# Kernel optimization log

Hardware: AMD Instinct MI355X
Metric: run time of the kernel (lower is better)

Reference implementation:

```python
import jax, jax.numpy as jnp
import numpy as np

EPS_COS = 1e-8
EPS_SHARP = 1e-16


def setup_inputs() -> dict:
    key = jax.random.key(0)
    k1, k2, k3, k4 = jax.random.split(key, 4)
    B, H, R, C, M = 512, 512, 2048, 64, 3
    out_dim = 3 * C + 2 * M + 4  # 202
    h = jax.random.normal(k1, (B, H), dtype=jnp.float32)
    prev_w = jax.random.uniform(k2, (B, R), dtype=jnp.float32)
    prev_w = prev_w / prev_w.sum(axis=1, keepdims=True)  # valid focus distribution
    memory = jax.random.normal(k3, (B, R, C), dtype=jnp.float32)
    fc_w = jax.random.normal(k4, (out_dim, H), dtype=jnp.float32) * 0.05
    fc_b = jnp.zeros((out_dim,), dtype=jnp.float32)
    return {"h": h, "prev_w": prev_w, "memory": memory, "fc_w": fc_w, "fc_b": fc_b}


def _write_head(h, prev_w, memory, fc_w, fc_b):
    B, R, C = memory.shape
    total = fc_w.shape[0]
    shift_len = total - 3 * C - 3          # 2*max_shift + 1
    m = (shift_len - 1) // 2               # max_shift

    z = h @ fc_w.T + fc_b                  # [B, total]
    sizes = [C, 1, 1, shift_len, 1, C, C]
    offs = np.cumsum([0] + sizes)
    k     = jnp.tanh(z[:, offs[0]:offs[1]])                 # [B, C]
    beta  = jax.nn.softplus(z[:, offs[1]:offs[2]])          # [B, 1]
    g     = jax.nn.sigmoid(z[:, offs[2]:offs[3]])           # [B, 1]
    s     = jax.nn.softmax(z[:, offs[3]:offs[4]], axis=1)   # [B, 2m+1]
    gamma = jax.nn.softplus(z[:, offs[4]:offs[5]]) + 1.0    # [B, 1]
    e     = jax.nn.sigmoid(z[:, offs[5]:offs[6]])           # [B, C]
    a     = jnp.tanh(z[:, offs[6]:offs[7]])                 # [B, C]

    # content addressing: cosine similarity of k vs each memory row
    num = jnp.einsum('bc,brc->br', k, memory)
    k_n = jnp.maximum(jnp.linalg.norm(k, axis=1, keepdims=True), EPS_COS)   # [B,1]
    m_n = jnp.maximum(jnp.linalg.norm(memory, axis=2), EPS_COS)             # [B,R]
    w_c = jax.nn.softmax(beta * (num / (k_n * m_n)), axis=1)                # [B,R]

    # gated interpolation
    w_g = g * w_c + (1.0 - g) * prev_w                                      # [B,R]

    # circular shift (per-sample cross-correlation, O(B*R*(2m+1)))
    unrolled = jnp.concatenate([w_g[:, -m:], w_g, w_g[:, :m]], axis=1)      # [B, R+2m]
    windows = jnp.stack([unrolled[:, j:j + R] for j in range(2 * m + 1)], axis=1)  # [B,2m+1,R]
    w_s = jnp.einsum('bjr,bj->br', windows, s)                              # [B,R]

    # sharpen
    w_p = jnp.power(w_s, gamma)
    w = w_p / (w_p.sum(axis=1, keepdims=True) + EPS_SHARP)                  # [B,R]

    # erase + write (fused)
    wE = w[:, :, None]                                                      # [B,R,1]
    new_mem = memory * (1.0 - wE * e[:, None, :]) + wE * a[:, None, :]      # [B,R,C]
    return w, new_mem


def reference(h, prev_w, memory, fc_w, fc_b):
    return _write_head(h, prev_w, memory, fc_w, fc_b)
```

## Files before the change

kernel.cpp:

```cpp
#include <hip/hip_runtime.h>
#include <math.h>

#define BB 512
#define HH 512
#define RR 2048
#define CC 64
#define OUTD 202
#define PSTRIDE 208
#define K_OFF 0
#define E_OFF 64
#define A_OFF 128
#define S_OFF 192
#define COMBO_OFF 199
#define G_OFF 200
#define GAMMA_OFF 201

#define PART_STRIDE 224

typedef float f32x4 __attribute__((ext_vector_type(4)));

__device__ __forceinline__ float softplusf_(float x) {
    return (x > 20.f) ? x : log1pf(expf(x));
}
__device__ __forceinline__ float sigmoidf_(float x) {
    return 1.f / (1.f + expf(-x));
}

__global__ __launch_bounds__(256) void params_part_kernel(
    const float* __restrict__ h, const float* __restrict__ fc_w,
    float* __restrict__ part)
{
    __shared__ float h_sh[8][128];
    const int tid = threadIdx.x;
    const int bg = blockIdx.x >> 2;
    const int hq = blockIdx.x & 3;
    const int b0 = bg * 8;
    const int h0 = hq * 128;

    for (int idx = tid; idx < 8 * 128; idx += 256) {
        int j = idx >> 7, i = idx & 127;
        h_sh[j][i] = h[(size_t)(b0 + j) * HH + h0 + i];
    }
    __syncthreads();

    if (tid < OUTD) {
        float acc[8];
        #pragma unroll
        for (int j = 0; j < 8; ++j) acc[j] = 0.f;
        const float4* wr = (const float4*)(fc_w + (size_t)tid * HH + h0);
        #pragma unroll 4
        for (int i4 = 0; i4 < 32; ++i4) {
            float4 wv = wr[i4];
            int i = i4 * 4;
            #pragma unroll
            for (int j = 0; j < 8; ++j) {
                acc[j] = fmaf(wv.x, h_sh[j][i + 0], acc[j]);
                acc[j] = fmaf(wv.y, h_sh[j][i + 1], acc[j]);
                acc[j] = fmaf(wv.z, h_sh[j][i + 2], acc[j]);
                acc[j] = fmaf(wv.w, h_sh[j][i + 3], acc[j]);
            }
        }
        #pragma unroll
        for (int j = 0; j < 8; ++j) {
            part[((size_t)(b0 + j) * 4 + hq) * PART_STRIDE + tid] = acc[j];
        }
    }
}

__global__ __launch_bounds__(256) void params_combine_kernel(
    const float* __restrict__ part, const float* __restrict__ fc_b,
    float* __restrict__ pw)
{
    __shared__ float z_sh[80];
    const int b = blockIdx.x;
    const int tid = threadIdx.x;
    float* p = pw + (size_t)b * PSTRIDE;

    if (tid < OUTD) {
        const float* q = part + (size_t)b * 4 * PART_STRIDE + tid;
        float z = q[0] + q[PART_STRIDE] + q[2 * PART_STRIDE]
                + q[3 * PART_STRIDE] + fc_b[tid];
        if (tid < 74) z_sh[tid] = z;
        if (tid < 64)                      p[K_OFF + tid] = tanhf(z);
        else if (tid == 65)                p[G_OFF] = sigmoidf_(z);
        else if (tid == 73)                p[GAMMA_OFF] = softplusf_(z) + 1.f;
        else if (tid >= 74 && tid < 138)   p[E_OFF + (tid - 74)] = sigmoidf_(z);
        else if (tid >= 138)               p[A_OFF + (tid - 138)] = tanhf(z);
    }
    __syncthreads();

    if (tid < 64) {
        float kv = tanhf(z_sh[tid]);
        float ss = kv * kv;
        #pragma unroll
        for (int m = 1; m < 64; m <<= 1) ss += __shfl_xor(ss, m, 64);
        if (tid == 0) {
            float kn = fmaxf(sqrtf(ss), 1e-8f);
            float beta = softplusf_(z_sh[64]);
            p[COMBO_OFF] = beta / kn;
            float mx = -1e30f;
            #pragma unroll
            for (int q = 0; q < 7; ++q) mx = fmaxf(mx, z_sh[66 + q]);
            float ev[7], se = 0.f;
            #pragma unroll
            for (int q = 0; q < 7; ++q) {
                ev[q] = __expf(z_sh[66 + q] - mx);
                se += ev[q];
            }
            float inv = 1.f / se;
            #pragma unroll
            for (int q = 0; q < 7; ++q) p[S_OFF + q] = ev[q] * inv;
        }
    }
}

__device__ __forceinline__ float block_reduce_sum4(float v, float* red) {
    #pragma unroll
    for (int m = 1; m < 64; m <<= 1) v += __shfl_xor(v, m, 64);
    int wid = threadIdx.x >> 6;
    if ((threadIdx.x & 63) == 0) red[wid] = v;
    __syncthreads();
    float x = red[0] + red[1] + red[2] + red[3];
    __syncthreads();
    return x;
}

__global__ __launch_bounds__(256) void score_kernel(
    const float* __restrict__ memory, const float* __restrict__ pw,
    float* __restrict__ sc, float* __restrict__ esum)
{
    __shared__ float red[4];
    const int tid = threadIdx.x;
    const int b = blockIdx.x >> 2;
    const int rbase = (blockIdx.x & 3) * 512;
    const int lane16 = tid & 15;
    const int rgrp = tid >> 4;
    const float* p = pw + (size_t)b * PSTRIDE;
    const float4 k4 = *(const float4*)(p + K_OFF + lane16 * 4);
    const float combo = p[COMBO_OFF];
    const float* memb = memory + (size_t)b * RR * CC;

    float lsum = 0.f;
    #pragma unroll 8
    for (int i = 0; i < 32; ++i) {
        int r = rbase + i * 16 + rgrp;
        float4 m4 = *(const float4*)(memb + (size_t)r * CC + lane16 * 4);
        float num = m4.x * k4.x + m4.y * k4.y + m4.z * k4.z + m4.w * k4.w;
        float ssq = m4.x * m4.x + m4.y * m4.y + m4.z * m4.z + m4.w * m4.w;
        #pragma unroll
        for (int m = 1; m < 16; m <<= 1) {
            num += __shfl_xor(num, m, 64);
            ssq += __shfl_xor(ssq, m, 64);
        }
        if (lane16 == 0) {
            float mn = fmaxf(sqrtf(ssq), 1e-8f);
            float ev = __expf(combo * num / mn);
            sc[(size_t)b * RR + r] = ev;
            lsum += ev;
        }
    }
    float bs = block_reduce_sum4(lsum, red);
    if (tid == 0) esum[blockIdx.x] = bs;
}

__device__ __forceinline__ float block_reduce_sum16(float v, float* red) {
    #pragma unroll
    for (int m = 1; m < 64; m <<= 1) v += __shfl_xor(v, m, 64);
    int wid = threadIdx.x >> 6;
    if ((threadIdx.x & 63) == 0) red[wid] = v;
    __syncthreads();
    if (threadIdx.x < 16) {
        float x = red[threadIdx.x];
        #pragma unroll
        for (int m = 1; m < 16; m <<= 1) x += __shfl_xor(x, m, 64);
        if (threadIdx.x == 0) red[0] = x;
    }
    __syncthreads();
    float r = red[0];
    __syncthreads();
    return r;
}

__global__ __launch_bounds__(1024) void wu_kernel(
    const float* __restrict__ memory, const float* __restrict__ sc,
    const float* __restrict__ esum, const float* __restrict__ prev_w,
    const float* __restrict__ pw, float* __restrict__ out_w,
    float* __restrict__ out_mem)
{
    __shared__ float wg[RR];
    __shared__ float wps[RR];
    __shared__ float red[16];

    const int b = blockIdx.x;
    const int tid = threadIdx.x;
    const float* p = pw + (size_t)b * PSTRIDE;
    const float g = p[G_OFF];
    const float gamma = p[GAMMA_OFF];
    const float s0 = p[S_OFF + 0], s1 = p[S_OFF + 1], s2 = p[S_OFF + 2],
                s3 = p[S_OFF + 3], s4 = p[S_OFF + 4], s5 = p[S_OFF + 5],
                s6 = p[S_OFF + 6];
    const float* eb = esum + (size_t)b * 4;
    const float se = eb[0] + eb[1] + eb[2] + eb[3];
    const float gi = g / se, omg = 1.f - g;

    {
        const int r2 = tid * 2;
        float2 ev = *(const float2*)(sc + (size_t)b * RR + r2);
        float2 pv = *(const float2*)(prev_w + (size_t)b * RR + r2);
        wg[r2]     = gi * ev.x + omg * pv.x;
        wg[r2 + 1] = gi * ev.y + omg * pv.y;
    }
    __syncthreads();

    float lp = 0.f;
    {
        const int r2 = tid * 2;
        #pragma unroll
        for (int q = 0; q < 2; ++q) {
            int r = r2 + q;
            float acc = s0 * wg[(r - 3) & (RR - 1)]
                      + s1 * wg[(r - 2) & (RR - 1)]
                      + s2 * wg[(r - 1) & (RR - 1)]
                      + s3 * wg[r]
                      + s4 * wg[(r + 1) & (RR - 1)]
                      + s5 * wg[(r + 2) & (RR - 1)]
                      + s6 * wg[(r + 3) & (RR - 1)];
            float v = __powf(acc, gamma);
            wps[r] = v;
            lp += v;
        }
    }
    const float ps = block_reduce_sum16(lp, red);
    const float invp = 1.f / (ps + 1e-16f);

    {
        const int r2 = tid * 2;
        float w0 = wps[r2] * invp;
        float w1 = wps[r2 + 1] * invp;
        wg[r2] = w0;
        wg[r2 + 1] = w1;
        *(float2*)(out_w + (size_t)b * RR + r2) = make_float2(w0, w1);
    }
    __syncthreads();

    const int lane8 = tid & 7;
    const int rgrp = tid >> 3;
    const f32x4 ea = *(const f32x4*)(p + E_OFF + lane8 * 8);
    const f32x4 eb2 = *(const f32x4*)(p + E_OFF + lane8 * 8 + 4);
    const f32x4 aa = *(const f32x4*)(p + A_OFF + lane8 * 8);
    const f32x4 ab = *(const f32x4*)(p + A_OFF + lane8 * 8 + 4);
    const float* memb = memory + (size_t)b * RR * CC;
    float* omb = out_mem + (size_t)b * RR * CC;

    #pragma unroll
    for (int mi = 0; mi < 4; ++mi) {
        f32x4 ma[4], mb[4];
        float wv[4];
        #pragma unroll
        for (int j = 0; j < 4; ++j) {
            int r = (mi * 4 + j) * 128 + rgrp;
            const f32x4* mp = (const f32x4*)(memb + (size_t)r * CC + lane8 * 8);
            ma[j] = mp[0];
            mb[j] = mp[1];
            wv[j] = wg[r];
        }
        #pragma unroll
        for (int j = 0; j < 4; ++j) {
            int r = (mi * 4 + j) * 128 + rgrp;
            f32x4 oa, ob;
            oa.x = ma[j].x * (1.f - wv[j] * ea.x) + wv[j] * aa.x;
            oa.y = ma[j].y * (1.f - wv[j] * ea.y) + wv[j] * aa.y;
            oa.z = ma[j].z * (1.f - wv[j] * ea.z) + wv[j] * aa.z;
            oa.w = ma[j].w * (1.f - wv[j] * ea.w) + wv[j] * aa.w;
            ob.x = mb[j].x * (1.f - wv[j] * eb2.x) + wv[j] * ab.x;
            ob.y = mb[j].y * (1.f - wv[j] * eb2.y) + wv[j] * ab.y;
            ob.z = mb[j].z * (1.f - wv[j] * eb2.z) + wv[j] * ab.z;
            ob.w = mb[j].w * (1.f - wv[j] * eb2.w) + wv[j] * ab.w;
            f32x4* op = (f32x4*)(omb + (size_t)r * CC + lane8 * 8);
            op[0] = oa;
            op[1] = ob;
        }
    }
}

extern "C" void kernel_launch(void* const* d_in, const int* in_sizes, int n_in,
                              void* d_out, int out_size, void* d_ws, size_t ws_size,
                              hipStream_t stream) {
    const float* h      = (const float*)d_in[0];
    const float* prev_w = (const float*)d_in[1];
    const float* memory = (const float*)d_in[2];
    const float* fc_w   = (const float*)d_in[3];
    const float* fc_b   = (const float*)d_in[4];

    float* pw      = (float*)d_ws;
    float* out_w   = (float*)d_out;
    float* out_mem = out_w + (size_t)BB * RR;

    const size_t pw_f   = (size_t)BB * PSTRIDE;
    const size_t br_f   = (size_t)BB * RR;
    const size_t es_f   = (size_t)BB * 4;
    const size_t part_f = (size_t)BB * 4 * PART_STRIDE;
    const size_t need_f = pw_f + br_f + es_f + part_f;

    float* sc   = pw + pw_f;
    float* esum = sc + br_f;
    float* part = esum + es_f;

    if (ws_size >= need_f * sizeof(float)) {
        params_part_kernel<<<256, 256, 0, stream>>>(h, fc_w, part);
        params_combine_kernel<<<BB, 256, 0, stream>>>(part, fc_b, pw);
        score_kernel<<<BB * 4, 256, 0, stream>>>(memory, pw, sc, esum);
        wu_kernel<<<BB, 1024, 0, stream>>>(memory, sc, esum, prev_w, pw,
                                           out_w, out_mem);
    } else {
        float* sc_fb   = out_mem;
        float* esum_fb = pw + pw_f;
        float* part_fb = esum_fb + es_f;
        params_part_kernel<<<256, 256, 0, stream>>>(h, fc_w, part_fb);
        params_combine_kernel<<<BB, 256, 0, stream>>>(part_fb, fc_b, pw);
        score_kernel<<<BB * 4, 256, 0, stream>>>(memory, pw, sc_fb, esum_fb);
        wu_kernel<<<BB, 1024, 0, stream>>>(memory, sc_fb, esum_fb, prev_w, pw,
                                           out_w, out_mem);
    }
}
```

Before: 191.4 us.

## Split fused weight/update kernel into separate weight and memory-update kernels

Splits the fused per-sample kernel in two. A 256-thread kernel computes the shifted, sharpened weights and writes them to the output. A second kernel runs over four row-blocks per sample and applies the erase/write update, reading the weights from global memory. The goal is more blocks and better occupancy for the bandwidth-bound memory update, instead of every 1024-thread block stalling on the serial weight phase first. The update grid is launched in reverse block order, so it likely reuses memory rows still in cache from the score kernel. The cost is one extra launch and a small global round-trip for the weights.

```diff
diff --git a/kernel.cpp b/kernel.cpp
--- a/kernel.cpp
+++ b/kernel.cpp
@@ -163,34 +163,14 @@
     if (tid == 0) esum[blockIdx.x] = bs;
 }
 
-__device__ __forceinline__ float block_reduce_sum16(float v, float* red) {
-    #pragma unroll
-    for (int m = 1; m < 64; m <<= 1) v += __shfl_xor(v, m, 64);
-    int wid = threadIdx.x >> 6;
-    if ((threadIdx.x & 63) == 0) red[wid] = v;
-    __syncthreads();
-    if (threadIdx.x < 16) {
-        float x = red[threadIdx.x];
-        #pragma unroll
-        for (int m = 1; m < 16; m <<= 1) x += __shfl_xor(x, m, 64);
-        if (threadIdx.x == 0) red[0] = x;
-    }
-    __syncthreads();
-    float r = red[0];
-    __syncthreads();
-    return r;
-}
-
-__global__ __launch_bounds__(1024) void wu_kernel(
-    const float* __restrict__ memory, const float* __restrict__ sc,
-    const float* __restrict__ esum, const float* __restrict__ prev_w,
-    const float* __restrict__ pw, float* __restrict__ out_w,
-    float* __restrict__ out_mem)
-{
+__global__ __launch_bounds__(256) void weight_kernel(
+    const float* __restrict__ sc, const float* __restrict__ esum,
+    const float* __restrict__ prev_w, const float* __restrict__ pw,
+    float* __restrict__ out_w)
+{
+    __shared__ float buf[RR];
     __shared__ float wg[RR];
-    __shared__ float wps[RR];
-    __shared__ float red[16];
-
+    __shared__ float red[4];
     const int b = blockIdx.x;
     const int tid = threadIdx.x;
     const float* p = pw + (size_t)b * PSTRIDE;
@@ -203,8 +183,9 @@
     const float se = eb[0] + eb[1] + eb[2] + eb[3];
     const float gi = g / se, omg = 1.f - g;
 
-    {
-        const int r2 = tid * 2;
+    #pragma unroll
+    for (int t = 0; t < 4; ++t) {
+        int r2 = (t * 256 + tid) * 2;
         float2 ev = *(const float2*)(sc + (size_t)b * RR + r2);
         float2 pv = *(const float2*)(prev_w + (size_t)b * RR + r2);
         wg[r2]     = gi * ev.x + omg * pv.x;
@@ -213,44 +194,49 @@
     __syncthreads();
 
     float lp = 0.f;
-    {
-        const int r2 = tid * 2;
-        #pragma unroll
-        for (int q = 0; q < 2; ++q) {
-            int r = r2 + q;
-            float acc = s0 * wg[(r - 3) & (RR - 1)]
-                      + s1 * wg[(r - 2) & (RR - 1)]
-                      + s2 * wg[(r - 1) & (RR - 1)]
-                      + s3 * wg[r]
-                      + s4 * wg[(r + 1) & (RR - 1)]
-                      + s5 * wg[(r + 2) & (RR - 1)]
-                      + s6 * wg[(r + 3) & (RR - 1)];
-            float v = __powf(acc, gamma);
-            wps[r] = v;
-            lp += v;
-        }
-    }
-    const float ps = block_reduce_sum16(lp, red);
+    #pragma unroll
+    for (int t = 0; t < 8; ++t) {
+        int r = t * 256 + tid;
+        float acc = s0 * wg[(r - 3) & (RR - 1)]
+                  + s1 * wg[(r - 2) & (RR - 1)]
+                  + s2 * wg[(r - 1) & (RR - 1)]
+                  + s3 * wg[r]
+                  + s4 * wg[(r + 1) & (RR - 1)]
+                  + s5 * wg[(r + 2) & (RR - 1)]
+                  + s6 * wg[(r + 3) & (RR - 1)];
+        float v = __powf(acc, gamma);
+        buf[r] = v;
+        lp += v;
+    }
+    const float ps = block_reduce_sum4(lp, red);
     const float invp = 1.f / (ps + 1e-16f);
 
-    {
-        const int r2 = tid * 2;
-        float w0 = wps[r2] * invp;
-        float w1 = wps[r2 + 1] * invp;
-        wg[r2] = w0;
-        wg[r2 + 1] = w1;
-        *(float2*)(out_w + (size_t)b * RR + r2) = make_float2(w0, w1);
-    }
-    __syncthreads();
-
+    #pragma unroll
+    for (int t = 0; t < 4; ++t) {
+        int r2 = (t * 256 + tid) * 2;
+        *(float2*)(out_w + (size_t)b * RR + r2) =
+            make_float2(buf[r2] * invp, buf[r2 + 1] * invp);
+    }
+}
+
+__global__ __launch_bounds__(256) void update_kernel(
+    const float* __restrict__ memory, const float* __restrict__ w,
+    const float* __restrict__ pw, float* __restrict__ out_mem)
+{
+    const int bid = (int)gridDim.x - 1 - (int)blockIdx.x;
+    const int b = bid >> 2;
+    const int rbase = (bid & 3) * 512;
+    const int tid = threadIdx.x;
     const int lane8 = tid & 7;
     const int rgrp = tid >> 3;
+    const float* p = pw + (size_t)b * PSTRIDE;
     const f32x4 ea = *(const f32x4*)(p + E_OFF + lane8 * 8);
     const f32x4 eb2 = *(const f32x4*)(p + E_OFF + lane8 * 8 + 4);
     const f32x4 aa = *(const f32x4*)(p + A_OFF + lane8 * 8);
     const f32x4 ab = *(const f32x4*)(p + A_OFF + lane8 * 8 + 4);
     const float* memb = memory + (size_t)b * RR * CC;
     float* omb = out_mem + (size_t)b * RR * CC;
+    const float* wb = w + (size_t)b * RR;
 
     #pragma unroll
     for (int mi = 0; mi < 4; ++mi) {
@@ -258,15 +244,15 @@
         float wv[4];
         #pragma unroll
         for (int j = 0; j < 4; ++j) {
-            int r = (mi * 4 + j) * 128 + rgrp;
+            int r = rbase + (mi * 4 + j) * 32 + rgrp;
             const f32x4* mp = (const f32x4*)(memb + (size_t)r * CC + lane8 * 8);
             ma[j] = mp[0];
             mb[j] = mp[1];
-            wv[j] = wg[r];
+            wv[j] = wb[r];
         }
         #pragma unroll
         for (int j = 0; j < 4; ++j) {
-            int r = (mi * 4 + j) * 128 + rgrp;
+            int r = rbase + (mi * 4 + j) * 32 + rgrp;
             f32x4 oa, ob;
             oa.x = ma[j].x * (1.f - wv[j] * ea.x) + wv[j] * aa.x;
             oa.y = ma[j].y * (1.f - wv[j] * ea.y) + wv[j] * aa.y;
@@ -310,8 +296,8 @@
         params_part_kernel<<<256, 256, 0, stream>>>(h, fc_w, part);
         params_combine_kernel<<<BB, 256, 0, stream>>>(part, fc_b, pw);
         score_kernel<<<BB * 4, 256, 0, stream>>>(memory, pw, sc, esum);
-        wu_kernel<<<BB, 1024, 0, stream>>>(memory, sc, esum, prev_w, pw,
-                                           out_w, out_mem);
+        weight_kernel<<<BB, 256, 0, stream>>>(sc, esum, prev_w, pw, out_w);
+        update_kernel<<<BB * 4, 256, 0, stream>>>(memory, out_w, pw, out_mem);
     } else {
         float* sc_fb   = out_mem;
         float* esum_fb = pw + pw_f;
@@ -319,7 +305,7 @@
         params_part_kernel<<<256, 256, 0, stream>>>(h, fc_w, part_fb);
         params_combine_kernel<<<BB, 256, 0, stream>>>(part_fb, fc_b, pw);
         score_kernel<<<BB * 4, 256, 0, stream>>>(memory, pw, sc_fb, esum_fb);
-        wu_kernel<<<BB, 1024, 0, stream>>>(memory, sc_fb, esum_fb, prev_w, pw,
-                                           out_w, out_mem);
-    }
-}
+        weight_kernel<<<BB, 256, 0, stream>>>(sc_fb, esum_fb, prev_w, pw, out_w);
+        update_kernel<<<BB * 4, 256, 0, stream>>>(memory, out_w, pw, out_mem);
+    }
+}
```

New measurement: 188.8 us (median of 2 runs). About the same (-1.4%).
